# Kernel tuning notes

Measured on AMD Instinct MI355X. Metric: run time of the kernel, lower is better.

## Reference

```python
import jax, jax.numpy as jnp
import numpy as np

HEAD_SIZE = 64

def setup_inputs() -> dict:
    key = jax.random.key(0)
    k1, k2, k3, k4 = jax.random.split(key, 4)
    B, T, D = 4, 4096, 768
    x = jax.random.normal(k1, (B, T, D), dtype=jnp.float32)
    Wq = jax.random.normal(k2, (D, HEAD_SIZE), dtype=jnp.float32) * (1.0 / np.sqrt(D))
    Wk = jax.random.normal(k3, (D, HEAD_SIZE), dtype=jnp.float32) * (1.0 / np.sqrt(D))
    Wv = jax.random.normal(k4, (D, HEAD_SIZE), dtype=jnp.float32) * (1.0 / np.sqrt(D))
    return {"x": x, "Wq": Wq, "Wk": Wk, "Wv": Wv}

def reference(x, Wq, Wk, Wv):
    # q,k,v: [B, T, H]
    q = jnp.einsum('btd,dh->bth', x, Wq)
    k = jnp.einsum('btd,dh->bth', x, Wk)
    v = jnp.einsum('btd,dh->bth', x, Wv)
    # scores: [B, T, T]; causal mask via lower-triangular band, -inf elsewhere
    scores = jnp.einsum('bqh,bkh->bqk', q, k)
    T = x.shape[1]
    causal = jnp.tril(jnp.ones((T, T), dtype=bool))  # band_part(ones, -1, 0)
    scores = jnp.where(causal[None, :, :], scores, -jnp.inf)
    attn = jax.nn.softmax(scores / np.sqrt(HEAD_SIZE), axis=-1)
    # dropout is identity in eval mode
    return jnp.einsum('bqk,bkh->bqh', attn, v)
```

## Files before the change

### kernel.cpp

```cpp
#include <hip/hip_runtime.h>
#include <math.h>

typedef __attribute__((ext_vector_type(8))) short short8;
typedef __attribute__((ext_vector_type(4))) float f32x4;
typedef unsigned short ushort_t;

#define TSEQ   4096
#define NBATCH 4
#define DMODEL 768
#define HS     64
#define KSPLIT 4

static __device__ __forceinline__ ushort_t f2bf(float f) {
  union { float f; unsigned u; } v; v.f = f;
  unsigned r = v.u + 0x7fffu + ((v.u >> 16) & 1u);
  return (ushort_t)(r >> 16);
}
static __device__ __forceinline__ float bf2f(ushort_t u) {
  union { unsigned u; float f; } v; v.u = ((unsigned)u) << 16; return v.f;
}

#define MFMA16(a,b,c) __builtin_amdgcn_mfma_f32_16x16x32_bf16((a),(b),(c),0,0,0)

__global__ __launch_bounds__(256) void wprep(
    const float* __restrict__ Wq, const float* __restrict__ Wk,
    const float* __restrict__ Wv, ushort_t* __restrict__ Wt)
{
  __shared__ float lds[64 * 65];
  const int m = blockIdx.x / 12, kc = blockIdx.x % 12, k0 = kc * 64;
  const float* W = (m == 0) ? Wq : (m == 1) ? Wk : Wv;
  const int tid = threadIdx.x;
#pragma unroll
  for (int i = 0; i < 16; i++) {
    const int row = i * 4 + (tid >> 6), col = tid & 63;
    lds[row * 65 + col] = W[(size_t)(k0 + row) * HS + col];
  }
  __syncthreads();
#pragma unroll
  for (int i = 0; i < 16; i++) {
    const int n = i * 4 + (tid >> 6), kk = tid & 63;
    Wt[(size_t)(m * 64 + n) * DMODEL + k0 + kk] = f2bf(lds[kk * 65 + n]);
  }
}

__global__ __launch_bounds__(256, 2) void qkv_mfma(
    const float* __restrict__ x, const ushort_t* __restrict__ Wt,
    ushort_t* __restrict__ q, ushort_t* __restrict__ kO, ushort_t* __restrict__ vT)
{
  __shared__ __align__(16) ushort_t Abuf[2][32 * 72];

  const int tid  = threadIdx.x;
  const int w    = tid >> 6, lane = tid & 63;
  const int l16  = lane & 15, quad = lane >> 4;
  const int mh   = w >> 1, ns = w & 1;
  const int M0   = blockIdx.x * 32;
  const float* xg = x + (size_t)M0 * DMODEL;

  const int srow = tid >> 3, scol = (tid & 7) * 8;
  const float* xs = xg + (size_t)srow * DMODEL + scol;
  const ushort_t* wb = Wt + (size_t)(ns * 96 + l16) * DMODEL + quad * 8;

  f32x4 acc[6];
#pragma unroll
  for (int nt = 0; nt < 6; nt++) acc[nt] = (f32x4){0.f, 0.f, 0.f, 0.f};

  float4 pr0 = *(const float4*)(xs);
  float4 pr1 = *(const float4*)(xs + 4);
  short8 bpre[12];
#pragma unroll
  for (int nt = 0; nt < 6; nt++)
#pragma unroll
    for (int kc = 0; kc < 2; kc++)
      bpre[nt * 2 + kc] = *(const short8*)(wb + (size_t)nt * 16 * DMODEL + kc * 32);

  for (int ks = 0; ks < DMODEL / 64; ks++) {
    ushort_t* Ab = &Abuf[ks & 1][0];
    {
      short8 p;
      p[0]=f2bf(pr0.x); p[1]=f2bf(pr0.y); p[2]=f2bf(pr0.z); p[3]=f2bf(pr0.w);
      p[4]=f2bf(pr1.x); p[5]=f2bf(pr1.y); p[6]=f2bf(pr1.z); p[7]=f2bf(pr1.w);
      *(short8*)(Ab + srow * 72 + scol) = p;
    }
    if (ks < DMODEL / 64 - 1) {
      const float* xn = xs + (ks + 1) * 64;
      pr0 = *(const float4*)(xn);
      pr1 = *(const float4*)(xn + 4);
    }
    __syncthreads();
    short8 bcur[12];
#pragma unroll
    for (int t = 0; t < 12; t++) bcur[t] = bpre[t];
    if (ks < DMODEL / 64 - 1) {
#pragma unroll
      for (int nt = 0; nt < 6; nt++)
#pragma unroll
        for (int kc = 0; kc < 2; kc++)
          bpre[nt * 2 + kc] =
              *(const short8*)(wb + (size_t)nt * 16 * DMODEL + (ks + 1) * 64 + kc * 32);
    }
#pragma unroll
    for (int kc = 0; kc < 2; kc++) {
      const short8 af = *(const short8*)(Ab + (mh * 16 + l16) * 72 + kc * 32 + quad * 8);
#pragma unroll
      for (int nt = 0; nt < 6; nt++) acc[nt] = MFMA16(af, bcur[nt * 2 + kc], acc[nt]);
    }
  }

#pragma unroll
  for (int nt = 0; nt < 6; nt++) {
    const int gnt = ns * 6 + nt;
    const int mat = gnt >> 2;
    if (mat <= 1) {
      const int col = (gnt & 3) * 16 + l16;
#pragma unroll
      for (int r = 0; r < 4; r++) {
        const float val = acc[nt][r];
        const int trow = M0 + mh * 16 + quad * 4 + r;
        if (mat == 0) q [(size_t)trow * HS + col] = f2bf(val * 0.125f);
        else          kO[(size_t)trow * HS + col] = f2bf(val);
      }
    }
  }
  __syncthreads();
  float* vls = (float*)&Abuf[0][0];
  if (ns == 1) {
#pragma unroll
    for (int nt = 2; nt < 6; nt++) {
      const int vcol = ((ns * 6 + nt) & 3) * 16 + l16;
#pragma unroll
      for (int r = 0; r < 4; r++)
        vls[(mh * 16 + quad * 4 + r) * 65 + vcol] = acc[nt][r];
    }
  }
  __syncthreads();
  const int d = tid >> 2, seg = tid & 3;
  short8 pk;
#pragma unroll
  for (int i = 0; i < 8; i++) pk[i] = (short)f2bf(vls[(seg * 8 + i) * 65 + d]);
  *(short8*)(vT + ((size_t)(M0 >> 12) * HS + d) * TSEQ + (M0 & (TSEQ - 1)) + seg * 8) = pk;
}

#define KP 72
__global__ __launch_bounds__(128) void attn_part(
    const ushort_t* __restrict__ q, const ushort_t* __restrict__ k,
    const ushort_t* __restrict__ vT, float* __restrict__ ML, ushort_t* __restrict__ OP)
{
  __shared__ __align__(16) ushort_t sK[64 * KP];
  __shared__ __align__(16) ushort_t sV[64 * KP];
  __shared__ __align__(16) ushort_t sP[2][16 * KP];

  const int idx  = blockIdx.x;
  const int s    = idx & 3;
  const int b    = (idx >> 2) & 3;
  const int jt   = 127 - (idx >> 4);
  const int tid  = threadIdx.x;
  const int w    = tid >> 6;
  const int lane = tid & 63;
  const int l16  = lane & 15, quad = lane >> 4;
  const int R0   = jt * 32 + w * 16;

  const ushort_t* qg = q  + (size_t)b * TSEQ * HS;
  const ushort_t* kg = k  + (size_t)b * TSEQ * HS;
  const ushort_t* vg = vT + (size_t)b * HS * TSEQ;

  const short8 qf0 = *(const short8*)(qg + (R0 + l16) * HS +      quad * 8);
  const short8 qf1 = *(const short8*)(qg + (R0 + l16) * HS + 32 + quad * 8);

  f32x4 o[4];
#pragma unroll
  for (int dt = 0; dt < 4; dt++) o[dt] = (f32x4){0.f, 0.f, 0.f, 0.f};
  float mrow = -INFINITY, lrow = 0.f;

  const int nkt = jt / 2 + 1;
  short8 kpre[4], vpre[4];
  int kt = s;
  if (kt < nkt) {
    const int k0 = kt * 64;
#pragma unroll
    for (int i = 0; i < 4; i++) {
      const int c = i * 128 + tid, key = c >> 3, ch = c & 7;
      kpre[i] = *(const short8*)(kg + (size_t)(k0 + key) * HS + ch * 8);
      vpre[i] = *(const short8*)(vg + (size_t)key * TSEQ + k0 + ch * 8);
    }
  }
  for (; kt < nkt; kt += KSPLIT) {
    const int k0 = kt * 64;
    __syncthreads();
#pragma unroll
    for (int i = 0; i < 4; i++) {
      const int c = i * 128 + tid, key = c >> 3, ch = c & 7;
      *(short8*)(sK + key * KP + ch * 8) = kpre[i];
      *(short8*)(sV + key * KP + ch * 8) = vpre[i];
    }
    if (kt + KSPLIT < nkt) {
      const int kn = (kt + KSPLIT) * 64;
#pragma unroll
      for (int i = 0; i < 4; i++) {
        const int c = i * 128 + tid, key = c >> 3, ch = c & 7;
        kpre[i] = *(const short8*)(kg + (size_t)(kn + key) * HS + ch * 8);
        vpre[i] = *(const short8*)(vg + (size_t)key * TSEQ + kn + ch * 8);
      }
    }
    __syncthreads();
    f32x4 sT[4];
#pragma unroll
    for (int ct = 0; ct < 4; ct++) {
      sT[ct] = (f32x4){0.f, 0.f, 0.f, 0.f};
      const short8 kfa = *(const short8*)(sK + (ct * 16 + l16) * KP +      quad * 8);
      const short8 kfb = *(const short8*)(sK + (ct * 16 + l16) * KP + 32 + quad * 8);
      sT[ct] = MFMA16(kfa, qf0, sT[ct]);
      sT[ct] = MFMA16(kfb, qf1, sT[ct]);
    }
    if (k0 + 63 > R0) {
      const int qrow = R0 + l16;
#pragma unroll
      for (int ct = 0; ct < 4; ct++)
#pragma unroll
        for (int r = 0; r < 4; r++)
          sT[ct][r] = (k0 + ct * 16 + quad * 4 + r <= qrow) ? sT[ct][r] : -INFINITY;
    }
    float tm = -INFINITY;
#pragma unroll
    for (int ct = 0; ct < 4; ct++)
#pragma unroll
      for (int r = 0; r < 4; r++) tm = fmaxf(tm, sT[ct][r]);
    tm = fmaxf(tm, __shfl_xor(tm, 16));
    tm = fmaxf(tm, __shfl_xor(tm, 32));
    const float mn = fmaxf(mrow, tm);
    const float al = __expf(mrow - mn);
    mrow = mn;
    float ps = 0.f;
#pragma unroll
    for (int ct = 0; ct < 4; ct++)
#pragma unroll
      for (int r = 0; r < 4; r++) { sT[ct][r] = __expf(sT[ct][r] - mn); ps += sT[ct][r]; }
    ps += __shfl_xor(ps, 16);
    ps += __shfl_xor(ps, 32);
    lrow = lrow * al + ps;
    ushort_t* Pw = &sP[w][0];
#pragma unroll
    for (int ct = 0; ct < 4; ct++) {
      ushort4 pk;
      pk.x = f2bf(sT[ct][0]); pk.y = f2bf(sT[ct][1]);
      pk.z = f2bf(sT[ct][2]); pk.w = f2bf(sT[ct][3]);
      *(ushort4*)(Pw + l16 * KP + ct * 16 + quad * 4) = pk;
    }
    float alo[4];
#pragma unroll
    for (int r = 0; r < 4; r++) alo[r] = __shfl(al, quad * 4 + r);
#pragma unroll
    for (int dt = 0; dt < 4; dt++)
#pragma unroll
      for (int r = 0; r < 4; r++) o[dt][r] *= alo[r];
    const short8 pf0 = *(const short8*)(Pw + l16 * KP +      quad * 8);
    const short8 pf1 = *(const short8*)(Pw + l16 * KP + 32 + quad * 8);
#pragma unroll
    for (int dt = 0; dt < 4; dt++) {
      const short8 vfa = *(const short8*)(sV + (dt * 16 + l16) * KP +      quad * 8);
      const short8 vfb = *(const short8*)(sV + (dt * 16 + l16) * KP + 32 + quad * 8);
      o[dt] = MFMA16(pf0, vfa, o[dt]);
      o[dt] = MFMA16(pf1, vfb, o[dt]);
    }
  }

  const size_t base = ((size_t)(b * KSPLIT + s) * TSEQ);
  if (quad == 0) {
    ML[(base + R0 + l16) * 2 + 0] = mrow;
    ML[(base + R0 + l16) * 2 + 1] = lrow;
  }
#pragma unroll
  for (int dt = 0; dt < 4; dt++)
#pragma unroll
    for (int r = 0; r < 4; r++)
      OP[(base + R0 + quad * 4 + r) * HS + dt * 16 + l16] = f2bf(o[dt][r]);
}

__global__ __launch_bounds__(256) void attn_merge(
    const float* __restrict__ ML, const ushort_t* __restrict__ OP,
    float* __restrict__ out)
{
  const int row = blockIdx.x * 16 + (threadIdx.x >> 4);
  const int b   = row >> 12, t = row & (TSEQ - 1);
  const int d0  = (threadIdx.x & 15) * 4;
  float m[KSPLIT], l[KSPLIT];
  float M = -INFINITY;
#pragma unroll
  for (int ss = 0; ss < KSPLIT; ss++) {
    const size_t i = ((size_t)(b * KSPLIT + ss) * TSEQ + t);
    m[ss] = ML[i * 2]; l[ss] = ML[i * 2 + 1];
    M = fmaxf(M, m[ss]);
  }
  float den = 0.f;
  float4 num = make_float4(0.f, 0.f, 0.f, 0.f);
#pragma unroll
  for (int ss = 0; ss < KSPLIT; ss++) {
    const float a = __expf(m[ss] - M);
    den += l[ss] * a;
    const size_t i = ((size_t)(b * KSPLIT + ss) * TSEQ + t);
    const ushort4 u = *(const ushort4*)(OP + i * HS + d0);
    num.x += a * bf2f(u.x); num.y += a * bf2f(u.y);
    num.z += a * bf2f(u.z); num.w += a * bf2f(u.w);
  }
  const float inv = 1.f / den;
  *(float4*)(out + (size_t)row * HS + d0) =
      make_float4(num.x * inv, num.y * inv, num.z * inv, num.w * inv);
}

extern "C" void kernel_launch(void* const* d_in, const int* in_sizes, int n_in,
                              void* d_out, int out_size, void* d_ws, size_t ws_size,
                              hipStream_t stream) {
  const float* x  = (const float*)d_in[0];
  const float* Wq = (const float*)d_in[1];
  const float* Wk = (const float*)d_in[2];
  const float* Wv = (const float*)d_in[3];
  float* out = (float*)d_out;

  char* ws = (char*)d_ws;
  ushort_t* Wt = (ushort_t*)ws;
  ushort_t* qb = (ushort_t*)(ws + 294912);
  ushort_t* kb = (ushort_t*)(ws + 294912 + 2097152);
  ushort_t* vb = (ushort_t*)(ws + 294912 + 2 * 2097152);
  float*    ml = (float*)   (ws + 294912 + 3 * 2097152);
  ushort_t* op = (ushort_t*)(ws + 294912 + 3 * 2097152 + 524288);

  wprep<<<36, 256, 0, stream>>>(Wq, Wk, Wv, Wt);
  qkv_mfma<<<(NBATCH * TSEQ) / 32, 256, 0, stream>>>(x, Wt, qb, kb, vb);
  attn_part<<<128 * NBATCH * KSPLIT, 128, 0, stream>>>(qb, kb, vb, ml, op);
  attn_merge<<<1024, 256, 0, stream>>>(ml, op, out);
}
```

Measured before the change: 147.6 us.

## Load x fragments directly into registers in QKV projection, dropping LDS staging

Result: slower. 166.4 us (+12.7%).

```diff
diff --git a/kernel.cpp b/kernel.cpp
--- a/kernel.cpp
+++ b/kernel.cpp
@@ -43,101 +43,93 @@
   }
 }
 
-__global__ __launch_bounds__(256, 2) void qkv_mfma(
+__global__ __launch_bounds__(256, 4) void qkv_mfma(
     const float* __restrict__ x, const ushort_t* __restrict__ Wt,
     ushort_t* __restrict__ q, ushort_t* __restrict__ kO, ushort_t* __restrict__ vT)
 {
-  __shared__ __align__(16) ushort_t Abuf[2][32 * 72];
+  __shared__ __align__(16) float vls[16 * 65];
 
   const int tid  = threadIdx.x;
-  const int w    = tid >> 6, lane = tid & 63;
+  const int ns   = tid >> 6;
+  const int lane = tid & 63;
   const int l16  = lane & 15, quad = lane >> 4;
-  const int mh   = w >> 1, ns = w & 1;
-  const int M0   = blockIdx.x * 32;
-  const float* xg = x + (size_t)M0 * DMODEL;
-
-  const int srow = tid >> 3, scol = (tid & 7) * 8;
-  const float* xs = xg + (size_t)srow * DMODEL + scol;
-  const ushort_t* wb = Wt + (size_t)(ns * 96 + l16) * DMODEL + quad * 8;
-
-  f32x4 acc[6];
-#pragma unroll
-  for (int nt = 0; nt < 6; nt++) acc[nt] = (f32x4){0.f, 0.f, 0.f, 0.f};
-
-  float4 pr0 = *(const float4*)(xs);
-  float4 pr1 = *(const float4*)(xs + 4);
-  short8 bpre[12];
-#pragma unroll
-  for (int nt = 0; nt < 6; nt++)
+  const int M0   = blockIdx.x * 16;
+
+  const float*    xr = x  + (size_t)(M0 + l16) * DMODEL + quad * 8;
+  const ushort_t* wb = Wt + (size_t)(ns * 48 + l16) * DMODEL + quad * 8;
+
+  f32x4 acc[3];
+#pragma unroll
+  for (int nt = 0; nt < 3; nt++) acc[nt] = (f32x4){0.f, 0.f, 0.f, 0.f};
+
+  float4 xp0 = *(const float4*)(xr);
+  float4 xp1 = *(const float4*)(xr + 4);
+  float4 xp2 = *(const float4*)(xr + 32);
+  float4 xp3 = *(const float4*)(xr + 36);
+  short8 bp[6];
+#pragma unroll
+  for (int nt = 0; nt < 3; nt++)
 #pragma unroll
     for (int kc = 0; kc < 2; kc++)
-      bpre[nt * 2 + kc] = *(const short8*)(wb + (size_t)nt * 16 * DMODEL + kc * 32);
+      bp[nt * 2 + kc] = *(const short8*)(wb + (size_t)nt * 16 * DMODEL + kc * 32);
 
   for (int ks = 0; ks < DMODEL / 64; ks++) {
-    ushort_t* Ab = &Abuf[ks & 1][0];
-    {
-      short8 p;
-      p[0]=f2bf(pr0.x); p[1]=f2bf(pr0.y); p[2]=f2bf(pr0.z); p[3]=f2bf(pr0.w);
-      p[4]=f2bf(pr1.x); p[5]=f2bf(pr1.y); p[6]=f2bf(pr1.z); p[7]=f2bf(pr1.w);
-      *(short8*)(Ab + srow * 72 + scol) = p;
-    }
+    const float4 xc0 = xp0, xc1 = xp1, xc2 = xp2, xc3 = xp3;
+    short8 bc[6];
+#pragma unroll
+    for (int t = 0; t < 6; t++) bc[t] = bp[t];
     if (ks < DMODEL / 64 - 1) {
-      const float* xn = xs + (ks + 1) * 64;
-      pr0 = *(const float4*)(xn);
-      pr1 = *(const float4*)(xn + 4);
-    }
-    __syncthreads();
-    short8 bcur[12];
-#pragma unroll
-    for (int t = 0; t < 12; t++) bcur[t] = bpre[t];
-    if (ks < DMODEL / 64 - 1) {
-#pragma unroll
-      for (int nt = 0; nt < 6; nt++)
+      const float* xn = xr + (ks + 1) * 64;
+      xp0 = *(const float4*)(xn);
+      xp1 = *(const float4*)(xn + 4);
+      xp2 = *(const float4*)(xn + 32);
+      xp3 = *(const float4*)(xn + 36);
+#pragma unroll
+      for (int nt = 0; nt < 3; nt++)
 #pragma unroll
         for (int kc = 0; kc < 2; kc++)
-          bpre[nt * 2 + kc] =
+          bp[nt * 2 + kc] =
               *(const short8*)(wb + (size_t)nt * 16 * DMODEL + (ks + 1) * 64 + kc * 32);
     }
-#pragma unroll
-    for (int kc = 0; kc < 2; kc++) {
-      const short8 af = *(const short8*)(Ab + (mh * 16 + l16) * 72 + kc * 32 + quad * 8);
-#pragma unroll
-      for (int nt = 0; nt < 6; nt++) acc[nt] = MFMA16(af, bcur[nt * 2 + kc], acc[nt]);
-    }
-  }
-
-#pragma unroll
-  for (int nt = 0; nt < 6; nt++) {
-    const int gnt = ns * 6 + nt;
+    short8 a0, a1;
+    a0[0] = f2bf(xc0.x); a0[1] = f2bf(xc0.y); a0[2] = f2bf(xc0.z); a0[3] = f2bf(xc0.w);
+    a0[4] = f2bf(xc1.x); a0[5] = f2bf(xc1.y); a0[6] = f2bf(xc1.z); a0[7] = f2bf(xc1.w);
+    a1[0] = f2bf(xc2.x); a1[1] = f2bf(xc2.y); a1[2] = f2bf(xc2.z); a1[3] = f2bf(xc2.w);
+    a1[4] = f2bf(xc3.x); a1[5] = f2bf(xc3.y); a1[6] = f2bf(xc3.z); a1[7] = f2bf(xc3.w);
+#pragma unroll
+    for (int nt = 0; nt < 3; nt++) {
+      acc[nt] = MFMA16(a0, bc[nt * 2 + 0], acc[nt]);
+      acc[nt] = MFMA16(a1, bc[nt * 2 + 1], acc[nt]);
+    }
+  }
+
+#pragma unroll
+  for (int nt = 0; nt < 3; nt++) {
+    const int gnt = ns * 3 + nt;
     const int mat = gnt >> 2;
-    if (mat <= 1) {
-      const int col = (gnt & 3) * 16 + l16;
-#pragma unroll
-      for (int r = 0; r < 4; r++) {
-        const float val = acc[nt][r];
-        const int trow = M0 + mh * 16 + quad * 4 + r;
-        if (mat == 0) q [(size_t)trow * HS + col] = f2bf(val * 0.125f);
-        else          kO[(size_t)trow * HS + col] = f2bf(val);
-      }
+    const int col = (gnt & 3) * 16 + l16;
+    if (mat == 0) {
+#pragma unroll
+      for (int r = 0; r < 4; r++)
+        q[(size_t)(M0 + quad * 4 + r) * HS + col] = f2bf(acc[nt][r] * 0.125f);
+    } else if (mat == 1) {
+#pragma unroll
+      for (int r = 0; r < 4; r++)
+        kO[(size_t)(M0 + quad * 4 + r) * HS + col] = f2bf(acc[nt][r]);
+    } else {
+#pragma unroll
+      for (int r = 0; r < 4; r++)
+        vls[(quad * 4 + r) * 65 + col] = acc[nt][r];
     }
   }
   __syncthreads();
-  float* vls = (float*)&Abuf[0][0];
-  if (ns == 1) {
-#pragma unroll
-    for (int nt = 2; nt < 6; nt++) {
-      const int vcol = ((ns * 6 + nt) & 3) * 16 + l16;
-#pragma unroll
-      for (int r = 0; r < 4; r++)
-        vls[(mh * 16 + quad * 4 + r) * 65 + vcol] = acc[nt][r];
-    }
-  }
-  __syncthreads();
-  const int d = tid >> 2, seg = tid & 3;
-  short8 pk;
-#pragma unroll
-  for (int i = 0; i < 8; i++) pk[i] = (short)f2bf(vls[(seg * 8 + i) * 65 + d]);
-  *(short8*)(vT + ((size_t)(M0 >> 12) * HS + d) * TSEQ + (M0 & (TSEQ - 1)) + seg * 8) = pk;
+  if (tid < 128) {
+    const int d = tid >> 1, seg = tid & 1;
+    short8 pk;
+#pragma unroll
+    for (int i = 0; i < 8; i++) pk[i] = (short)f2bf(vls[(seg * 8 + i) * 65 + d]);
+    *(short8*)(vT + ((size_t)(M0 >> 12) * HS + d) * TSEQ + (M0 & (TSEQ - 1)) + seg * 8) = pk;
+  }
 }
 
 #define KP 72
@@ -324,7 +316,7 @@
   ushort_t* op = (ushort_t*)(ws + 294912 + 3 * 2097152 + 524288);
 
   wprep<<<36, 256, 0, stream>>>(Wq, Wk, Wv, Wt);
-  qkv_mfma<<<(NBATCH * TSEQ) / 32, 256, 0, stream>>>(x, Wt, qb, kb, vb);
+  qkv_mfma<<<(NBATCH * TSEQ) / 16, 256, 0, stream>>>(x, Wt, qb, kb, vb);
   attn_part<<<128 * NBATCH * KSPLIT, 128, 0, stream>>>(qb, kb, vb, ml, op);
   attn_merge<<<1024, 256, 0, stream>>>(ml, op, out);
 }
```
